# Kernel optimization log

Hardware: AMD Instinct MI355X
Metric: run time of the kernel (lower is better)

The kernel has to match this reference:

```python
import jax, jax.numpy as jnp
import numpy as np

V, DM, DEPTH, N = 50257, 512, 8, 16  # vocab, dim, depth, ssm_dim
B, L = 2, 1024
GATE = 0.5  # fixed_gate=True blend


def layer_norm(x, g, b):
    mu = x.mean(-1, keepdims=True)
    xm = x - mu
    var = (xm * xm).mean(-1, keepdims=True)
    return xm * jax.lax.rsqrt(var + 1e-5) * g + b


def ssm(u, W_dt, b_dt, W_B, W_C, A_log, D_p):
    # selective SSM: h_t = exp(dt_t*A)*h_{t-1} + dt_t*B_t*u_t ; y_t = C_t.h_t + D*u_t
    dt = jax.nn.softplus(u @ W_dt + b_dt)            # (B,L,DM)
    Bm = u @ W_B                                      # (B,L,N)
    Cm = u @ W_C                                      # (B,L,N)
    A = -jnp.exp(A_log)                               # (DM,N), stable (negative)

    def step(h, inp):
        dt_t, B_t, C_t, u_t = inp                     # (B,DM),(B,N),(B,N),(B,DM)
        h = jnp.exp(dt_t[..., None] * A) * h + (dt_t * u_t)[..., None] * B_t[:, None, :]
        y = jnp.einsum('bdn,bn->bd', h, C_t)
        return h, y

    h0 = jnp.zeros((u.shape[0], DM, N), u.dtype)
    xs = (dt.transpose(1, 0, 2), Bm.transpose(1, 0, 2), Cm.transpose(1, 0, 2), u.transpose(1, 0, 2))
    _, ys = jax.lax.scan(step, h0, xs)
    return ys.transpose(1, 0, 2) + D_p * u


def wkv(x, W_r, W_k, W_v, W_o, t_decay, t_first):
    # RWKV-4 channel-wise WKV recurrence
    r = jax.nn.sigmoid(x @ W_r)
    k = jnp.clip(x @ W_k, -30.0, 30.0)
    v = x @ W_v
    w = jnp.exp(-jnp.exp(t_decay))                    # (DM,) decay in (0,1)

    def step(carry, inp):
        a, b = carry
        k_t, v_t = inp
        ek = jnp.exp(k_t)
        eu = jnp.exp(t_first + k_t)
        out = (a + eu * v_t) / (b + eu + 1e-6)
        return (w * a + ek * v_t, w * b + ek), out

    a0 = jnp.zeros((x.shape[0], DM), x.dtype)
    _, o = jax.lax.scan(step, (a0, jnp.zeros_like(a0)), (k.transpose(1, 0, 2), v.transpose(1, 0, 2)))
    return (r * o.transpose(1, 0, 2)) @ W_o


def setup_inputs() -> dict:
    key = jax.random.key(0)
    ks = jax.random.split(key, 16)
    s = 0.02
    inp = {
        'input_ids': jax.random.randint(ks[0], (B, L), 0, V, dtype=jnp.int32),
        'emb': jax.random.normal(ks[1], (V, DM), jnp.float32) * s,
        'ln1_g': jnp.ones((DEPTH, DM), jnp.float32),
        'ln1_b': jnp.zeros((DEPTH, DM), jnp.float32),
        'W_dt': jax.random.normal(ks[2], (DEPTH, DM, DM), jnp.float32) * s,
        'b_dt': jnp.zeros((DEPTH, DM), jnp.float32),
        'W_B': jax.random.normal(ks[3], (DEPTH, DM, N), jnp.float32) * s,
        'W_C': jax.random.normal(ks[4], (DEPTH, DM, N), jnp.float32) * s,
        'A_log': jnp.broadcast_to(jnp.log(jnp.arange(1, N + 1, dtype=jnp.float32)), (DEPTH, DM, N)).copy(),
        'D_p': jnp.ones((DEPTH, DM), jnp.float32),
        'ln2_g': jnp.ones((DEPTH, DM), jnp.float32),
        'ln2_b': jnp.zeros((DEPTH, DM), jnp.float32),
        'W_r': jax.random.normal(ks[5], (DEPTH, DM, DM), jnp.float32) * s,
        'W_k': jax.random.normal(ks[6], (DEPTH, DM, DM), jnp.float32) * s,
        'W_v': jax.random.normal(ks[7], (DEPTH, DM, DM), jnp.float32) * s,
        'W_o': jax.random.normal(ks[8], (DEPTH, DM, DM), jnp.float32) * s,
        't_decay': jax.random.normal(ks[9], (DEPTH, DM), jnp.float32) * 0.5,
        't_first': jax.random.normal(ks[10], (DEPTH, DM), jnp.float32) * 0.5,
        'lnf_g': jnp.ones((DM,), jnp.float32),
        'lnf_b': jnp.zeros((DM,), jnp.float32),
    }
    return inp


def reference(input_ids, emb, ln1_g, ln1_b, W_dt, b_dt, W_B, W_C, A_log, D_p,
              ln2_g, ln2_b, W_r, W_k, W_v, W_o, t_decay, t_first, lnf_g, lnf_b):
    x = emb[input_ids]                                # (B,L,DM)
    for i in range(DEPTH):
        x = x + GATE * ssm(layer_norm(x, ln1_g[i], ln1_b[i]),
                           W_dt[i], b_dt[i], W_B[i], W_C[i], A_log[i], D_p[i])
        x = x + GATE * wkv(layer_norm(x, ln2_g[i], ln2_b[i]),
                           W_r[i], W_k[i], W_v[i], W_o[i], t_decay[i], t_first[i])
    x = layer_norm(x, lnf_g, lnf_b)
    logits = x @ emb.T                                # tied LM head, (B,L,V)
    return logits
```

## Files before the change

kernel.cpp:

```cpp
#include <hip/hip_runtime.h>

#define DM 512
#define NST 16
#define NDEPTH 8
#define NB 2
#define NL 1024
#define MROWS 2048
#define VOCAB 50257
#define VPAD  50304
#define NCH 64
#define CLEN 16

typedef __attribute__((ext_vector_type(8))) short bf16x8;
typedef __attribute__((ext_vector_type(4))) float f32x4;
typedef __attribute__((ext_vector_type(8))) unsigned short ushort8;

#define AS1(p) ((const __attribute__((address_space(1))) void*)(p))
#define AS3(p) ((__attribute__((address_space(3))) void*)(p))

static __device__ __forceinline__ unsigned short f2bf(float f) {
  unsigned int x = __float_as_uint(f);
  unsigned int r = (x + 0x7FFFu + ((x >> 16) & 1u)) >> 16;
  return (unsigned short)r;
}

__global__ __launch_bounds__(256) void k_gather(const int* __restrict__ ids,
    const float* __restrict__ emb, float* __restrict__ x)
{
  int gid = blockIdx.x * 256 + threadIdx.x;
  int row = gid >> 7, c = (gid & 127) * 4;
  int id = ids[row];
  *(float4*)(x + (size_t)row * DM + c) = *(const float4*)(emb + (size_t)id * DM + c);
}

__global__ void k_transpose(const float* __restrict__ Wdt, const float* __restrict__ Wr,
    const float* __restrict__ Wk, const float* __restrict__ Wv, const float* __restrict__ Wo,
    unsigned short* __restrict__ Tdtbc, unsigned short* __restrict__ Trkv, unsigned short* __restrict__ To)
{
  __shared__ float tile[32][33];
  int z = blockIdx.z, layer = z / 5, f = z % 5;
  const float* src;
  unsigned short* dst;
  size_t lw = (size_t)layer * DM * DM;
  if (f == 0)      { src = Wdt + lw; dst = Tdtbc + (size_t)layer * 640 * DM; }
  else if (f == 1) { src = Wr  + lw; dst = Trkv + (size_t)layer * 3 * DM * DM; }
  else if (f == 2) { src = Wk  + lw; dst = Trkv + (size_t)layer * 3 * DM * DM + DM * DM; }
  else if (f == 3) { src = Wv  + lw; dst = Trkv + (size_t)layer * 3 * DM * DM + 2 * DM * DM; }
  else             { src = Wo  + lw; dst = To   + lw; }
  int tx = threadIdx.x, ty = threadIdx.y;
  int kb = blockIdx.y * 32, nb = blockIdx.x * 32;
  #pragma unroll
  for (int i = 0; i < 4; i++)
    tile[ty + i * 8][tx] = src[(size_t)(kb + ty + i * 8) * DM + nb + tx];
  __syncthreads();
  #pragma unroll
  for (int i = 0; i < 4; i++)
    dst[(size_t)(nb + ty + i * 8) * DM + kb + tx] = f2bf(tile[tx][ty + i * 8]);
}

__global__ __launch_bounds__(256) void k_bcpack(const float* __restrict__ WB,
    const float* __restrict__ WC, unsigned short* __restrict__ Tdtbc)
{
  int gid = blockIdx.x * 256 + threadIdx.x;
  int k = gid & 511, n = (gid >> 9) & 127, layer = gid >> 16;
  float v = 0.f;
  if (n < 16)      v = WB[((size_t)layer * DM + k) * NST + n];
  else if (n < 32) v = WC[((size_t)layer * DM + k) * NST + (n - 16)];
  Tdtbc[(size_t)layer * 640 * DM + (size_t)(512 + n) * DM + k] = f2bf(v);
}

__global__ __launch_bounds__(256) void k_embcvt(const float* __restrict__ emb,
    unsigned short* __restrict__ out)
{
  int gid = blockIdx.x * 256 + threadIdx.x;
  size_t base = (size_t)gid * 8;
  int row = (int)(base >> 9);
  ushort8 o;
  if (row < VOCAB) {
    float4 a = *(const float4*)(emb + base);
    float4 b = *(const float4*)(emb + base + 4);
    o[0]=f2bf(a.x); o[1]=f2bf(a.y); o[2]=f2bf(a.z); o[3]=f2bf(a.w);
    o[4]=f2bf(b.x); o[5]=f2bf(b.y); o[6]=f2bf(b.z); o[7]=f2bf(b.w);
  } else {
    o = (ushort8)0;
  }
  *(ushort8*)(out + base) = o;
}

__global__ __launch_bounds__(256) void k_ln(const float* __restrict__ x,
    const float* __restrict__ g, const float* __restrict__ bb,
    float* __restrict__ of, unsigned short* __restrict__ ob)
{
  const int w = threadIdx.x >> 6, l = threadIdx.x & 63;
  const int row = blockIdx.x * 4 + w;
  const float* xr = x + (size_t)row * DM + l * 8;
  float4 v0 = *(const float4*)(xr);
  float4 v1 = *(const float4*)(xr + 4);
  float s = v0.x + v0.y + v0.z + v0.w + v1.x + v1.y + v1.z + v1.w;
  float q = v0.x*v0.x + v0.y*v0.y + v0.z*v0.z + v0.w*v0.w
          + v1.x*v1.x + v1.y*v1.y + v1.z*v1.z + v1.w*v1.w;
  #pragma unroll
  for (int m = 1; m < 64; m <<= 1) { s += __shfl_xor(s, m); q += __shfl_xor(q, m); }
  const float mu = s * (1.0f / DM);
  const float var = q * (1.0f / DM) - mu * mu;
  const float rs = rsqrtf(var + 1e-5f);
  const float4 g0 = *(const float4*)(g + l * 8);
  const float4 g1 = *(const float4*)(g + l * 8 + 4);
  const float4 b0 = *(const float4*)(bb + l * 8);
  const float4 b1 = *(const float4*)(bb + l * 8 + 4);
  float y[8];
  y[0] = (v0.x - mu) * rs * g0.x + b0.x;
  y[1] = (v0.y - mu) * rs * g0.y + b0.y;
  y[2] = (v0.z - mu) * rs * g0.z + b0.z;
  y[3] = (v0.w - mu) * rs * g0.w + b0.w;
  y[4] = (v1.x - mu) * rs * g1.x + b1.x;
  y[5] = (v1.y - mu) * rs * g1.y + b1.y;
  y[6] = (v1.z - mu) * rs * g1.z + b1.z;
  y[7] = (v1.w - mu) * rs * g1.w + b1.w;
  if (of) {
    float4 o0 = {y[0], y[1], y[2], y[3]}, o1 = {y[4], y[5], y[6], y[7]};
    *(float4*)(of + (size_t)row * DM + l * 8) = o0;
    *(float4*)(of + (size_t)row * DM + l * 8 + 4) = o1;
  }
  if (ob) {
    ushort8 o;
    #pragma unroll
    for (int j = 0; j < 8; j++) o[j] = f2bf(y[j]);
    *(ushort8*)(ob + (size_t)row * DM + l * 8) = o;
  }
}

template<int BM, int BN, int EPI, bool SWZ>
__global__ __launch_bounds__(256) void gemm_bt(const unsigned short* __restrict__ A,
    const unsigned short* __restrict__ Bt, float* __restrict__ C, int N, int ldc,
    const float* __restrict__ bias, float* __restrict__ C2)
{
  constexpr int K = DM;
  constexpr int MI = BM / 32, NI = BN / 32;
  __shared__ unsigned short lsA[BM * 64];
  __shared__ unsigned short lsB[BN * 64];
  const int t = threadIdx.x;
  const int w = t >> 6, l = t & 63;
  const int wm = (w >> 1) * (BM / 2), wn = (w & 1) * (BN / 2);
  size_t bm, bn;
  if constexpr (SWZ) {
    const int per = gridDim.x >> 3;
    const int wg = ((int)blockIdx.x & 7) * per + ((int)blockIdx.x >> 3);
    bm = (size_t)(wg & 15) * BM; bn = (size_t)(wg >> 4) * BN;
  } else {
    bm = (size_t)blockIdx.x * BM; bn = (size_t)blockIdx.y * BN;
  }
  f32x4 acc[MI][NI] = {};
  const int srow = t >> 3, sslot = t & 7;
  const int gs = sslot ^ (srow & 7);
  const unsigned short* Ag = A + (bm + srow) * K + gs * 8;
  const unsigned short* Bg = Bt + (bn + srow) * K + gs * 8;
  const int lr = l & 15, lq = l >> 4;
  for (int k0 = 0; k0 < K; k0 += 64) {
    #pragma unroll
    for (int o = 0; o < BM / 32; ++o)
      __builtin_amdgcn_global_load_lds(AS1(Ag + (size_t)(o * 32) * K + k0),
          AS3(lsA + (o * 32 + srow) * 64 + sslot * 8), 16, 0, 0);
    #pragma unroll
    for (int o = 0; o < BN / 32; ++o)
      __builtin_amdgcn_global_load_lds(AS1(Bg + (size_t)(o * 32) * K + k0),
          AS3(lsB + (o * 32 + srow) * 64 + sslot * 8), 16, 0, 0);
    asm volatile("s_waitcnt vmcnt(0)" ::: "memory");
    __syncthreads();
    bf16x8 af[MI][2], bfr[NI][2];
    #pragma unroll
    for (int i = 0; i < MI; ++i) {
      int row = wm + i * 16 + lr;
      #pragma unroll
      for (int h = 0; h < 2; ++h)
        af[i][h] = *(const bf16x8*)(lsA + row * 64 + (((h * 4 + lq) ^ (row & 7)) * 8));
    }
    #pragma unroll
    for (int i = 0; i < NI; ++i) {
      int row = wn + i * 16 + lr;
      #pragma unroll
      for (int h = 0; h < 2; ++h)
        bfr[i][h] = *(const bf16x8*)(lsB + row * 64 + (((h * 4 + lq) ^ (row & 7)) * 8));
    }
    #pragma unroll
    for (int h = 0; h < 2; ++h)
      #pragma unroll
      for (int mi = 0; mi < MI; ++mi)
        #pragma unroll
        for (int ni = 0; ni < NI; ++ni)
          acc[mi][ni] = __builtin_amdgcn_mfma_f32_16x16x32_bf16(af[mi][h], bfr[ni][h], acc[mi][ni], 0, 0, 0);
    __syncthreads();
  }
  const int lg = l >> 4;
  #pragma unroll
  for (int mi = 0; mi < MI; ++mi) {
    #pragma unroll
    for (int ni = 0; ni < NI; ++ni) {
      int n = (int)bn + wn + ni * 16 + lr;
      if (EPI == 4 && n >= N) continue;
      size_t m0 = bm + wm + mi * 16 + lg * 4;
      #pragma unroll
      for (int j = 0; j < 4; ++j) {
        float v = acc[mi][ni][j];
        if (EPI == 0 || EPI == 4) {
          C[(m0 + j) * (size_t)ldc + n] = v;
        } else if (EPI == 2) {
          C2[(m0 + j) * (size_t)ldc + n] += 0.5f * v;
        } else {
          if (n < 512) {
            float b = v + bias[n];
            C[(m0 + j) * (size_t)512 + n] = fmaxf(b, 0.f) + log1pf(__expf(-fabsf(b)));
          } else if (n < 544) {
            C2[(m0 + j) * (size_t)32 + (n - 512)] = v;
          }
        }
      }
    }
  }
}

__global__ __launch_bounds__(256) void k_ssm1(const float* __restrict__ dt,
    const float* __restrict__ u, const float* __restrict__ BC,
    const float* __restrict__ A_log, float* __restrict__ Pb, float* __restrict__ Sb)
{
  const int t = threadIdx.x;
  const int grp = t >> 4, n = t & 15;
  const int cg = blockIdx.x & 63, ck = blockIdx.x >> 6;
  const int ch = cg * 16 + grp;
  const int b = ch >> 9, d = ch & 511;
  const float A = -__expf(A_log[d * NST + n]);
  const int t0 = ck * CLEN;
  const float* dtp = dt + ((size_t)b * NL + t0) * DM + d;
  const float* up  = u  + ((size_t)b * NL + t0) * DM + d;
  const float* bcp = BC + ((size_t)b * NL + t0) * 32 + n;
  float P = 1.f, S = 0.f;
  #pragma unroll
  for (int tt = 0; tt < CLEN; ++tt) {
    float dtv = dtp[(size_t)tt * DM];
    float uv  = up[(size_t)tt * DM];
    float Bv  = bcp[(size_t)tt * 32];
    float e = __expf(dtv * A);
    S = fmaf(e, S, dtv * uv * Bv);
    P *= e;
  }
  size_t cn = (size_t)ch * NST + n;
  Pb[cn * NCH + ck] = P;
  Sb[cn * NCH + ck] = S;
}

__global__ __launch_bounds__(256) void k_ssm2(const float* __restrict__ Pb,
    const float* __restrict__ Sb, float* __restrict__ H0)
{
  const int wid = blockIdx.x * 4 + (threadIdx.x >> 6);
  const int lane = threadIdx.x & 63;
  float coef = Pb[(size_t)wid * NCH + lane];
  float sum  = Sb[(size_t)wid * NCH + lane];
  #pragma unroll
  for (int m = 1; m < 64; m <<= 1) {
    float cr = __shfl_up(coef, m);
    float sr = __shfl_up(sum, m);
    if (lane >= m) { sum = fmaf(coef, sr, sum); coef *= cr; }
  }
  float hp = __shfl_up(sum, 1);
  H0[(size_t)wid * NCH + lane] = (lane == 0) ? 0.f : hp;
}

__global__ __launch_bounds__(256) void k_ssm3(const float* __restrict__ dt,
    const float* __restrict__ u, const float* __restrict__ BC,
    const float* __restrict__ A_log, const float* __restrict__ Dp,
    const float* __restrict__ H0, float* __restrict__ x)
{
  const int t = threadIdx.x;
  const int grp = t >> 4, n = t & 15;
  const int cg = blockIdx.x & 63, ck = blockIdx.x >> 6;
  const int ch = cg * 16 + grp;
  const int b = ch >> 9, d = ch & 511;
  const float A = -__expf(A_log[d * NST + n]);
  const float Dpv = Dp[d];
  const int t0 = ck * CLEN;
  const float* dtp = dt + ((size_t)b * NL + t0) * DM + d;
  const float* up  = u  + ((size_t)b * NL + t0) * DM + d;
  const float* bcp = BC + ((size_t)b * NL + t0) * 32 + n;
  float* xp = x + ((size_t)b * NL + t0) * DM + d;
  size_t cn = (size_t)ch * NST + n;
  float h = H0[cn * NCH + ck];
  #pragma unroll
  for (int tt = 0; tt < CLEN; ++tt) {
    float dtv = dtp[(size_t)tt * DM];
    float uv  = up[(size_t)tt * DM];
    float Bv  = bcp[(size_t)tt * 32];
    float Cv  = bcp[(size_t)tt * 32 + 16];
    float e = __expf(dtv * A);
    h = fmaf(e, h, dtv * uv * Bv);
    float p2 = h * Cv;
    p2 += __shfl_xor(p2, 1);
    p2 += __shfl_xor(p2, 2);
    p2 += __shfl_xor(p2, 4);
    p2 += __shfl_xor(p2, 8);
    if (n == 0) xp[(size_t)tt * DM] += 0.5f * (p2 + Dpv * uv);
  }
}

__global__ __launch_bounds__(256) void k_wkv1(const float* __restrict__ rkv,
    const float* __restrict__ tdec, float* __restrict__ SaB, float* __restrict__ SbB)
{
  const int gid = blockIdx.x * 256 + threadIdx.x;
  const int ch = gid & 1023, ck = gid >> 10;
  const int b = ch >> 9, d = ch & 511;
  const float w = __expf(-__expf(tdec[d]));
  const float* base = rkv + ((size_t)b * NL + ck * CLEN) * 1536;
  float Sa = 0.f, Sb = 0.f;
  #pragma unroll
  for (int tt = 0; tt < CLEN; ++tt) {
    const float* row = base + (size_t)tt * 1536;
    float kt = row[512 + d];
    kt = fminf(30.f, fmaxf(-30.f, kt));
    float vt = row[1024 + d];
    float ek = __expf(kt);
    Sa = fmaf(w, Sa, ek * vt);
    Sb = fmaf(w, Sb, ek);
  }
  SaB[(size_t)ch * NCH + ck] = Sa;
  SbB[(size_t)ch * NCH + ck] = Sb;
}

__global__ __launch_bounds__(256) void k_wkv2(const float* __restrict__ SaB,
    const float* __restrict__ SbB, const float* __restrict__ tdec,
    float* __restrict__ HaB, float* __restrict__ HbB)
{
  const int ch = blockIdx.x * 4 + (threadIdx.x >> 6);
  const int lane = threadIdx.x & 63;
  const int d = ch & 511;
  float coef = __expf(-16.f * __expf(tdec[d]));
  float sa = SaB[(size_t)ch * NCH + lane];
  float sb = SbB[(size_t)ch * NCH + lane];
  #pragma unroll
  for (int m = 1; m < 64; m <<= 1) {
    float cr  = __shfl_up(coef, m);
    float sar = __shfl_up(sa, m);
    float sbr = __shfl_up(sb, m);
    if (lane >= m) { sa = fmaf(coef, sar, sa); sb = fmaf(coef, sbr, sb); coef *= cr; }
  }
  float ha = __shfl_up(sa, 1);
  float hb = __shfl_up(sb, 1);
  HaB[(size_t)ch * NCH + lane] = (lane == 0) ? 0.f : ha;
  HbB[(size_t)ch * NCH + lane] = (lane == 0) ? 0.f : hb;
}

__global__ __launch_bounds__(256) void k_wkv3(const float* __restrict__ rkv,
    const float* __restrict__ tdec, const float* __restrict__ tfir,
    const float* __restrict__ HaB, const float* __restrict__ HbB,
    unsigned short* __restrict__ ro)
{
  const int gid = blockIdx.x * 256 + threadIdx.x;
  const int ch = gid & 1023, ck = gid >> 10;
  const int b = ch >> 9, d = ch & 511;
  const float w = __expf(-__expf(tdec[d]));
  const float tf = tfir[d];
  float a = HaB[(size_t)ch * NCH + ck];
  float bden = HbB[(size_t)ch * NCH + ck];
  const int t0 = ck * CLEN;
  const float* base = rkv + ((size_t)b * NL + t0) * 1536;
  unsigned short* rop = ro + ((size_t)b * NL + t0) * DM + d;
  #pragma unroll
  for (int tt = 0; tt < CLEN; ++tt) {
    const float* row = base + (size_t)tt * 1536;
    float rv = row[d];
    float kt = row[512 + d];
    kt = fminf(30.f, fmaxf(-30.f, kt));
    float vt = row[1024 + d];
    float ek = __expf(kt);
    float eu = __expf(tf + kt);
    float out = __fdividef(a + eu * vt, bden + eu + 1e-6f);
    float sig = __fdividef(1.f, 1.f + __expf(-rv));
    rop[(size_t)tt * DM] = f2bf(sig * out);
    a = fmaf(w, a, ek * vt);
    bden = fmaf(w, bden, ek);
  }
}

extern "C" void kernel_launch(void* const* d_in, const int* in_sizes, int n_in,
                              void* d_out, int out_size, void* d_ws, size_t ws_size,
                              hipStream_t stream)
{
  const int*   ids   = (const int*)d_in[0];
  const float* emb   = (const float*)d_in[1];
  const float* ln1_g = (const float*)d_in[2];
  const float* ln1_b = (const float*)d_in[3];
  const float* W_dt  = (const float*)d_in[4];
  const float* b_dt  = (const float*)d_in[5];
  const float* W_B   = (const float*)d_in[6];
  const float* W_C   = (const float*)d_in[7];
  const float* A_log = (const float*)d_in[8];
  const float* D_p   = (const float*)d_in[9];
  const float* ln2_g = (const float*)d_in[10];
  const float* ln2_b = (const float*)d_in[11];
  const float* W_r   = (const float*)d_in[12];
  const float* W_k   = (const float*)d_in[13];
  const float* W_v   = (const float*)d_in[14];
  const float* W_o   = (const float*)d_in[15];
  const float* t_dec = (const float*)d_in[16];
  const float* t_fir = (const float*)d_in[17];
  const float* lnf_g = (const float*)d_in[18];
  const float* lnf_b = (const float*)d_in[19];

  char* p = (char*)d_ws;
  float*          xres  = (float*)(p + 0);
  float*          u32   = (float*)(p + 4194304);
  float*          dtb   = (float*)(p + 8388608);
  float*          rkv   = (float*)(p + 12582912);
  float*          BCb   = (float*)(p + 25165824);
  unsigned short* abuf  = (unsigned short*)(p + 25427968);
  unsigned short* Tdtbc = (unsigned short*)(p + 27525120);
  unsigned short* To    = (unsigned short*)(p + 32768000);
  unsigned short* Trkv  = (unsigned short*)(p + 36962304);
  unsigned short* Tem   = (unsigned short*)(p + 49545216);

  float* Pb  = rkv;
  float* Sb  = rkv + 1048576;
  float* H0  = rkv + 2097152;
  float* SaB = dtb;
  float* SbB = dtb + 65536;
  float* HaB = dtb + 131072;
  float* HbB = dtb + 196608;

  k_gather<<<1024, 256, 0, stream>>>(ids, emb, xres);
  k_transpose<<<dim3(16, 16, 40), dim3(32, 8), 0, stream>>>(W_dt, W_r, W_k, W_v, W_o, Tdtbc, Trkv, To);
  k_bcpack<<<2048, 256, 0, stream>>>(W_B, W_C, Tdtbc);
  k_embcvt<<<12576, 256, 0, stream>>>(emb, Tem);

  for (int i = 0; i < NDEPTH; ++i) {
    k_ln<<<512, 256, 0, stream>>>(xres, ln1_g + i * DM, ln1_b + i * DM, u32, abuf);
    gemm_bt<64, 128, 3, false><<<dim3(32, 5), 256, 0, stream>>>(abuf,
        Tdtbc + (size_t)i * 640 * DM, dtb, 640, 512, b_dt + i * DM, BCb);
    k_ssm1<<<4096, 256, 0, stream>>>(dtb, u32, BCb, A_log + (size_t)i * DM * NST, Pb, Sb);
    k_ssm2<<<4096, 256, 0, stream>>>(Pb, Sb, H0);
    k_ssm3<<<4096, 256, 0, stream>>>(dtb, u32, BCb, A_log + (size_t)i * DM * NST,
        D_p + i * DM, H0, xres);
    k_ln<<<512, 256, 0, stream>>>(xres, ln2_g + i * DM, ln2_b + i * DM, nullptr, abuf);
    gemm_bt<64, 128, 0, false><<<dim3(32, 12), 256, 0, stream>>>(abuf,
        Trkv + (size_t)i * 3 * DM * DM, rkv, 1536, 1536, nullptr, nullptr);
    k_wkv1<<<256, 256, 0, stream>>>(rkv, t_dec + i * DM, SaB, SbB);
    k_wkv2<<<256, 256, 0, stream>>>(SaB, SbB, t_dec + i * DM, HaB, HbB);
    k_wkv3<<<256, 256, 0, stream>>>(rkv, t_dec + i * DM, t_fir + i * DM, HaB, HbB, abuf);
    gemm_bt<64, 128, 2, false><<<dim3(32, 4), 256, 0, stream>>>(abuf,
        To + (size_t)i * DM * DM, nullptr, 512, 512, nullptr, xres);
  }

  k_ln<<<512, 256, 0, stream>>>(xres, lnf_g, lnf_b, nullptr, abuf);
  gemm_bt<128, 128, 4, true><<<6288, 256, 0, stream>>>(abuf, Tem, (float*)d_out,
      VOCAB, VOCAB, nullptr, nullptr);
}
```

Baseline: 1.170 ms.

## Add dedicated 256x128 LM-head GEMM and halve scan chunk count

Replaces the generic swizzled 128x128 LM-head GEMM with a dedicated 512-thread kernel that uses 256x128 tiles and an XCD-aware block mapping. The larger tiles improve operand reuse for the large vocab projection, and some blocks exit early at the grid tail. Separately, the chunked SSM and WKV scans move from 64 chunks of 16 steps to 32 chunks of 32 steps, with the carry scans switched to 32-lane shuffles. This lowers inter-chunk scan work and launch sizes but lengthens each thread's serial loop and reduces parallelism in the recurrence kernels.

```diff
diff --git a/kernel.cpp b/kernel.cpp
--- a/kernel.cpp
+++ b/kernel.cpp
@@ -8,8 +8,8 @@
 #define MROWS 2048
 #define VOCAB 50257
 #define VPAD  50304
-#define NCH 64
-#define CLEN 16
+#define NCH 32
+#define CLEN 32
 
 typedef __attribute__((ext_vector_type(8))) short bf16x8;
 typedef __attribute__((ext_vector_type(4))) float f32x4;
@@ -130,7 +130,7 @@
   }
 }
 
-template<int BM, int BN, int EPI, bool SWZ>
+template<int BM, int BN, int EPI>
 __global__ __launch_bounds__(256) void gemm_bt(const unsigned short* __restrict__ A,
     const unsigned short* __restrict__ Bt, float* __restrict__ C, int N, int ldc,
     const float* __restrict__ bias, float* __restrict__ C2)
@@ -142,14 +142,7 @@
   const int t = threadIdx.x;
   const int w = t >> 6, l = t & 63;
   const int wm = (w >> 1) * (BM / 2), wn = (w & 1) * (BN / 2);
-  size_t bm, bn;
-  if constexpr (SWZ) {
-    const int per = gridDim.x >> 3;
-    const int wg = ((int)blockIdx.x & 7) * per + ((int)blockIdx.x >> 3);
-    bm = (size_t)(wg & 15) * BM; bn = (size_t)(wg >> 4) * BN;
-  } else {
-    bm = (size_t)blockIdx.x * BM; bn = (size_t)blockIdx.y * BN;
-  }
+  const size_t bm = (size_t)blockIdx.x * BM, bn = (size_t)blockIdx.y * BN;
   f32x4 acc[MI][NI] = {};
   const int srow = t >> 3, sslot = t & 7;
   const int gs = sslot ^ (srow & 7);
@@ -197,12 +190,11 @@
     #pragma unroll
     for (int ni = 0; ni < NI; ++ni) {
       int n = (int)bn + wn + ni * 16 + lr;
-      if (EPI == 4 && n >= N) continue;
       size_t m0 = bm + wm + mi * 16 + lg * 4;
       #pragma unroll
       for (int j = 0; j < 4; ++j) {
         float v = acc[mi][ni][j];
-        if (EPI == 0 || EPI == 4) {
+        if (EPI == 0) {
           C[(m0 + j) * (size_t)ldc + n] = v;
         } else if (EPI == 2) {
           C2[(m0 + j) * (size_t)ldc + n] += 0.5f * v;
@@ -219,6 +211,74 @@
   }
 }
 
+__global__ __launch_bounds__(512) void gemm_head(const unsigned short* __restrict__ A,
+    const unsigned short* __restrict__ Bt, float* __restrict__ C)
+{
+  __shared__ unsigned short lsA[256 * 64];
+  __shared__ unsigned short lsB[128 * 64];
+  const int t = threadIdx.x;
+  const int w = t >> 6, l = t & 63;
+  const int wm = (w >> 1) * 64, wn = (w & 1) * 64;
+  const int c = (int)blockIdx.x & 7, j = (int)blockIdx.x >> 3;
+  const int ntile = c * 50 + (j >> 3), mtile = j & 7;
+  if (ntile >= 393) return;
+  const size_t bm = (size_t)mtile * 256, bn = (size_t)ntile * 128;
+  f32x4 acc[4][4] = {};
+  const int srow = t >> 3, sslot = t & 7;
+  const int gs = sslot ^ (srow & 7);
+  const unsigned short* Ag = A + (bm + srow) * DM + gs * 8;
+  const unsigned short* Bg = Bt + (bn + srow) * DM + gs * 8;
+  const int lr = l & 15, lq = l >> 4;
+  for (int k0 = 0; k0 < DM; k0 += 64) {
+    #pragma unroll
+    for (int o = 0; o < 4; ++o)
+      __builtin_amdgcn_global_load_lds(AS1(Ag + (size_t)(o * 64) * DM + k0),
+          AS3(lsA + (o * 64 + srow) * 64 + sslot * 8), 16, 0, 0);
+    #pragma unroll
+    for (int o = 0; o < 2; ++o)
+      __builtin_amdgcn_global_load_lds(AS1(Bg + (size_t)(o * 64) * DM + k0),
+          AS3(lsB + (o * 64 + srow) * 64 + sslot * 8), 16, 0, 0);
+    asm volatile("s_waitcnt vmcnt(0)" ::: "memory");
+    __syncthreads();
+    bf16x8 af[4][2], bfr[4][2];
+    #pragma unroll
+    for (int i = 0; i < 4; ++i) {
+      int row = wm + i * 16 + lr;
+      #pragma unroll
+      for (int h = 0; h < 2; ++h)
+        af[i][h] = *(const bf16x8*)(lsA + row * 64 + (((h * 4 + lq) ^ (row & 7)) * 8));
+    }
+    #pragma unroll
+    for (int i = 0; i < 4; ++i) {
+      int row = wn + i * 16 + lr;
+      #pragma unroll
+      for (int h = 0; h < 2; ++h)
+        bfr[i][h] = *(const bf16x8*)(lsB + row * 64 + (((h * 4 + lq) ^ (row & 7)) * 8));
+    }
+    #pragma unroll
+    for (int h = 0; h < 2; ++h)
+      #pragma unroll
+      for (int mi = 0; mi < 4; ++mi)
+        #pragma unroll
+        for (int ni = 0; ni < 4; ++ni)
+          acc[mi][ni] = __builtin_amdgcn_mfma_f32_16x16x32_bf16(af[mi][h], bfr[ni][h], acc[mi][ni], 0, 0, 0);
+    __syncthreads();
+  }
+  const int lg = l >> 4;
+  #pragma unroll
+  for (int mi = 0; mi < 4; ++mi) {
+    #pragma unroll
+    for (int ni = 0; ni < 4; ++ni) {
+      int n = (int)bn + wn + ni * 16 + lr;
+      if (n >= VOCAB) continue;
+      size_t m0 = bm + wm + mi * 16 + lg * 4;
+      #pragma unroll
+      for (int jj = 0; jj < 4; ++jj)
+        C[(m0 + jj) * (size_t)VOCAB + n] = acc[mi][ni][jj];
+    }
+  }
+}
+
 __global__ __launch_bounds__(256) void k_ssm1(const float* __restrict__ dt,
     const float* __restrict__ u, const float* __restrict__ BC,
     const float* __restrict__ A_log, float* __restrict__ Pb, float* __restrict__ Sb)
@@ -251,17 +311,17 @@
 __global__ __launch_bounds__(256) void k_ssm2(const float* __restrict__ Pb,
     const float* __restrict__ Sb, float* __restrict__ H0)
 {
-  const int wid = blockIdx.x * 4 + (threadIdx.x >> 6);
-  const int lane = threadIdx.x & 63;
+  const int wid = blockIdx.x * 8 + (threadIdx.x >> 5);
+  const int lane = threadIdx.x & 31;
   float coef = Pb[(size_t)wid * NCH + lane];
   float sum  = Sb[(size_t)wid * NCH + lane];
   #pragma unroll
-  for (int m = 1; m < 64; m <<= 1) {
-    float cr = __shfl_up(coef, m);
-    float sr = __shfl_up(sum, m);
+  for (int m = 1; m < 32; m <<= 1) {
+    float cr = __shfl_up(coef, m, 32);
+    float sr = __shfl_up(sum, m, 32);
     if (lane >= m) { sum = fmaf(coef, sr, sum); coef *= cr; }
   }
-  float hp = __shfl_up(sum, 1);
+  float hp = __shfl_up(sum, 1, 32);
   H0[(size_t)wid * NCH + lane] = (lane == 0) ? 0.f : hp;
 }
 
@@ -328,21 +388,21 @@
     const float* __restrict__ SbB, const float* __restrict__ tdec,
     float* __restrict__ HaB, float* __restrict__ HbB)
 {
-  const int ch = blockIdx.x * 4 + (threadIdx.x >> 6);
-  const int lane = threadIdx.x & 63;
+  const int ch = blockIdx.x * 8 + (threadIdx.x >> 5);
+  const int lane = threadIdx.x & 31;
   const int d = ch & 511;
-  float coef = __expf(-16.f * __expf(tdec[d]));
+  float coef = __expf(-32.f * __expf(tdec[d]));
   float sa = SaB[(size_t)ch * NCH + lane];
   float sb = SbB[(size_t)ch * NCH + lane];
   #pragma unroll
-  for (int m = 1; m < 64; m <<= 1) {
-    float cr  = __shfl_up(coef, m);
-    float sar = __shfl_up(sa, m);
-    float sbr = __shfl_up(sb, m);
+  for (int m = 1; m < 32; m <<= 1) {
+    float cr  = __shfl_up(coef, m, 32);
+    float sar = __shfl_up(sa, m, 32);
+    float sbr = __shfl_up(sb, m, 32);
     if (lane >= m) { sa = fmaf(coef, sar, sa); sb = fmaf(coef, sbr, sb); coef *= cr; }
   }
-  float ha = __shfl_up(sa, 1);
-  float hb = __shfl_up(sb, 1);
+  float ha = __shfl_up(sa, 1, 32);
+  float hb = __shfl_up(sb, 1, 32);
   HaB[(size_t)ch * NCH + lane] = (lane == 0) ? 0.f : ha;
   HbB[(size_t)ch * NCH + lane] = (lane == 0) ? 0.f : hb;
 }
@@ -417,12 +477,12 @@
   unsigned short* Tem   = (unsigned short*)(p + 49545216);
 
   float* Pb  = rkv;
-  float* Sb  = rkv + 1048576;
-  float* H0  = rkv + 2097152;
+  float* Sb  = rkv + 524288;
+  float* H0  = rkv + 1048576;
   float* SaB = dtb;
-  float* SbB = dtb + 65536;
-  float* HaB = dtb + 131072;
-  float* HbB = dtb + 196608;
+  float* SbB = dtb + 32768;
+  float* HaB = dtb + 65536;
+  float* HbB = dtb + 98304;
 
   k_gather<<<1024, 256, 0, stream>>>(ids, emb, xres);
   k_transpose<<<dim3(16, 16, 40), dim3(32, 8), 0, stream>>>(W_dt, W_r, W_k, W_v, W_o, Tdtbc, Trkv, To);
@@ -431,23 +491,22 @@
 
   for (int i = 0; i < NDEPTH; ++i) {
     k_ln<<<512, 256, 0, stream>>>(xres, ln1_g + i * DM, ln1_b + i * DM, u32, abuf);
-    gemm_bt<64, 128, 3, false><<<dim3(32, 5), 256, 0, stream>>>(abuf,
+    gemm_bt<64, 128, 3><<<dim3(32, 5), 256, 0, stream>>>(abuf,
         Tdtbc + (size_t)i * 640 * DM, dtb, 640, 512, b_dt + i * DM, BCb);
-    k_ssm1<<<4096, 256, 0, stream>>>(dtb, u32, BCb, A_log + (size_t)i * DM * NST, Pb, Sb);
-    k_ssm2<<<4096, 256, 0, stream>>>(Pb, Sb, H0);
-    k_ssm3<<<4096, 256, 0, stream>>>(dtb, u32, BCb, A_log + (size_t)i * DM * NST,
+    k_ssm1<<<2048, 256, 0, stream>>>(dtb, u32, BCb, A_log + (size_t)i * DM * NST, Pb, Sb);
+    k_ssm2<<<2048, 256, 0, stream>>>(Pb, Sb, H0);
+    k_ssm3<<<2048, 256, 0, stream>>>(dtb, u32, BCb, A_log + (size_t)i * DM * NST,
         D_p + i * DM, H0, xres);
     k_ln<<<512, 256, 0, stream>>>(xres, ln2_g + i * DM, ln2_b + i * DM, nullptr, abuf);
-    gemm_bt<64, 128, 0, false><<<dim3(32, 12), 256, 0, stream>>>(abuf,
+    gemm_bt<64, 128, 0><<<dim3(32, 12), 256, 0, stream>>>(abuf,
         Trkv + (size_t)i * 3 * DM * DM, rkv, 1536, 1536, nullptr, nullptr);
-    k_wkv1<<<256, 256, 0, stream>>>(rkv, t_dec + i * DM, SaB, SbB);
-    k_wkv2<<<256, 256, 0, stream>>>(SaB, SbB, t_dec + i * DM, HaB, HbB);
-    k_wkv3<<<256, 256, 0, stream>>>(rkv, t_dec + i * DM, t_fir + i * DM, HaB, HbB, abuf);
-    gemm_bt<64, 128, 2, false><<<dim3(32, 4), 256, 0, stream>>>(abuf,
+    k_wkv1<<<128, 256, 0, stream>>>(rkv, t_dec + i * DM, SaB, SbB);
+    k_wkv2<<<128, 256, 0, stream>>>(SaB, SbB, t_dec + i * DM, HaB, HbB);
+    k_wkv3<<<128, 256, 0, stream>>>(rkv, t_dec + i * DM, t_fir + i * DM, HaB, HbB, abuf);
+    gemm_bt<64, 128, 2><<<dim3(32, 4), 256, 0, stream>>>(abuf,
         To + (size_t)i * DM * DM, nullptr, 512, 512, nullptr, xres);
   }
 
   k_ln<<<512, 256, 0, stream>>>(xres, lnf_g, lnf_b, nullptr, abuf);
-  gemm_bt<128, 128, 4, true><<<6288, 256, 0, stream>>>(abuf, Tem, (float*)d_out,
-      VOCAB, VOCAB, nullptr, nullptr);
-}
+  gemm_head<<<3200, 512, 0, stream>>>(abuf, Tem, (float*)d_out);
+}
```

Result: faster. 1.120 ms (-4.3%).
